# Kernel tuning notes

Hardware: AMD Instinct MI355X
Metric: run time of the kernel (lower is better)

Reference implementation:

```python
import jax, jax.numpy as jnp
import numpy as np

L, H, F_IN, OUT = 6, 2048, 2048, 2048
LN_EPS = 1e-5


def setup_inputs() -> dict:
    key = jax.random.key(0)
    ks = jax.random.split(key, 10)
    bound = 1.0 / np.sqrt(H)
    u = lambda k, shape: jax.random.uniform(k, shape, jnp.float32, -bound, bound)
    return {
        "x": jax.random.normal(ks[0], (1, 1, F_IN), jnp.float32),
        "hidden": jax.random.normal(ks[1], (L, 1, H), jnp.float32),
        "w_ih": u(ks[2], (L, 3 * H, H)),   # layer0 input size == H by construction
        "w_hh": u(ks[3], (L, 3 * H, H)),
        "b_ih": u(ks[4], (L, 3 * H)),
        "b_hh": u(ks[5], (L, 3 * H)),
        "ln_gamma": jnp.ones((H,), jnp.float32),
        "ln_beta": jnp.zeros((H,), jnp.float32),
        "lin_w": u(ks[6], (OUT, H)),
        "lin_b": u(ks[7], (OUT,)),
    }


def _gru_stack(x_t, hidden, w_ih, w_hh, b_ih, b_hh):
    # x_t: [B, H]; hidden: [L, B, H]. PyTorch gate order: r, z, n.
    def layer(inp, params):
        wi, wh, bi, bh, h = params
        gi = (inp @ wi.T + bi).reshape(inp.shape[0], 3, -1)  # [B,3,H]
        gh = (h @ wh.T + bh).reshape(h.shape[0], 3, -1)
        r = jax.nn.sigmoid(gi[:, 0] + gh[:, 0])
        z = jax.nn.sigmoid(gi[:, 1] + gh[:, 1])
        n = jnp.tanh(gi[:, 2] + r * gh[:, 2])
        h_new = (1.0 - z) * n + z * h
        return h_new, h_new

    top, new_hidden = jax.lax.scan(layer, x_t, (w_ih, w_hh, b_ih, b_hh, hidden))
    return top, new_hidden  # [B,H], [L,B,H]


def reference(x, hidden, w_ih, w_hh, b_ih, b_hh, ln_gamma, ln_beta, lin_w, lin_b):
    x_t = x[:, -1, :]  # [B, F_in]; T=1 so this is the only step
    out, new_hidden = _gru_stack(x_t, hidden, w_ih, w_hh, b_ih, b_hh)
    # LayerNorm over last dim
    mu = jnp.mean(out, axis=-1, keepdims=True)
    var = jnp.mean(jnp.square(out - mu), axis=-1, keepdims=True)
    out = (out - mu) * jax.lax.rsqrt(var + LN_EPS) * ln_gamma + ln_beta
    pred = out @ lin_w.T + lin_b + x_t[:, :OUT]
    return pred, new_hidden
```

## Files before the change

kernel.cpp:

```cpp
#include <hip/hip_runtime.h>


constexpr int HID = 2048;
constexpr int NL  = 6;
constexpr int G3  = 3 * HID;

__device__ __forceinline__ float wave_sum(float s){
  #pragma unroll
  for(int off = 32; off; off >>= 1) s += __shfl_down(s, off, 64);
  return s;
}

__device__ __forceinline__ float dot_f32(const float* __restrict__ row,
                                         const float* __restrict__ v, int lane){
  const float4* r4 = (const float4*)row;
  const float4* v4 = (const float4*)v;
  float s = 0.f;
  #pragma unroll
  for(int it = 0; it < 8; ++it){
    int idx = lane + 64 * it;
    float4 w = r4[idx], a = v4[idx];
    s += w.x * a.x + w.y * a.y + w.z * a.z + w.w * a.w;
  }
  return s;
}

__global__ __launch_bounds__(384) void k_layer(
    const float* __restrict__ w_ih_l,
    const float* __restrict__ w_hh_l,
    const float* __restrict__ b_ih_l,
    const float* __restrict__ b_hh_l,
    const float* __restrict__ h_l,
    const float* __restrict__ inp,
    float* __restrict__ h_new_ws,
    float* __restrict__ h_new_out)
{
  int j    = blockIdx.x;
  int wave = threadIdx.x >> 6;
  int lane = threadIdx.x & 63;
  __shared__ float sums[6];
  float s;
  if(wave < 3){
    s = dot_f32(w_ih_l + (size_t)(wave * HID + j) * HID, inp, lane);
  } else {
    s = dot_f32(w_hh_l + (size_t)((wave - 3) * HID + j) * HID, h_l, lane);
  }
  s = wave_sum(s);
  if(lane == 0) sums[wave] = s;
  __syncthreads();
  if(threadIdx.x == 0){
    float gi_r = sums[0] + b_ih_l[j];
    float gi_z = sums[1] + b_ih_l[HID + j];
    float gi_n = sums[2] + b_ih_l[2 * HID + j];
    float gh_r = sums[3] + b_hh_l[j];
    float gh_z = sums[4] + b_hh_l[HID + j];
    float gh_n = sums[5] + b_hh_l[2 * HID + j];
    float r = 1.f / (1.f + __expf(-(gi_r + gh_r)));
    float z = 1.f / (1.f + __expf(-(gi_z + gh_z)));
    float n = tanhf(gi_n + r * gh_n);
    float hn = (1.f - z) * n + z * h_l[j];
    h_new_ws[j]  = hn;
    h_new_out[j] = hn;
  }
}

__global__ __launch_bounds__(256) void k_layernorm(
    const float* __restrict__ h,
    const float* __restrict__ gamma,
    const float* __restrict__ beta,
    float* __restrict__ out)
{
  __shared__ float rs[4], rs2[4];
  __shared__ float s_mu, s_istd;
  int wave = threadIdx.x >> 6, lane = threadIdx.x & 63;
  float s = 0.f, s2 = 0.f;
  for(int i = threadIdx.x; i < HID; i += 256){ float v = h[i]; s += v; s2 += v * v; }
  #pragma unroll
  for(int off = 32; off; off >>= 1){ s += __shfl_down(s, off, 64); s2 += __shfl_down(s2, off, 64); }
  if(lane == 0){ rs[wave] = s; rs2[wave] = s2; }
  __syncthreads();
  if(threadIdx.x == 0){
    float S  = rs[0] + rs[1] + rs[2] + rs[3];
    float S2 = rs2[0] + rs2[1] + rs2[2] + rs2[3];
    float m   = S * (1.f / HID);
    float var = S2 * (1.f / HID) - m * m;
    s_mu = m; s_istd = rsqrtf(var + 1e-5f);
  }
  __syncthreads();
  float mu = s_mu, istd = s_istd;
  for(int i = threadIdx.x; i < HID; i += 256){
    out[i] = (h[i] - mu) * istd * gamma[i] + beta[i];
  }
}

__global__ __launch_bounds__(256) void k_linear(
    const float* __restrict__ v,
    const float* __restrict__ lin_w,
    const float* __restrict__ lin_b,
    const float* __restrict__ x,
    float* __restrict__ pred)
{
  int o    = blockIdx.x * 4 + (threadIdx.x >> 6);
  int lane = threadIdx.x & 63;
  float s = dot_f32(lin_w + (size_t)o * HID, v, lane);
  s = wave_sum(s);
  if(lane == 0) pred[o] = s + lin_b[o] + x[o];
}

extern "C" void kernel_launch(void* const* d_in, const int* in_sizes, int n_in,
                              void* d_out, int out_size, void* d_ws, size_t ws_size,
                              hipStream_t stream){
  const float* x      = (const float*)d_in[0];
  const float* hidden = (const float*)d_in[1];
  const float* w_ih   = (const float*)d_in[2];
  const float* w_hh   = (const float*)d_in[3];
  const float* b_ih   = (const float*)d_in[4];
  const float* b_hh   = (const float*)d_in[5];
  const float* gamma  = (const float*)d_in[6];
  const float* beta   = (const float*)d_in[7];
  const float* lin_w  = (const float*)d_in[8];
  const float* lin_b  = (const float*)d_in[9];
  float* out = (float*)d_out;

  float* buf = (float*)d_ws;

  for(int l = 0; l < NL; ++l){
    k_layer<<<HID, 384, 0, stream>>>(
        w_ih + (size_t)l * G3 * HID,
        w_hh + (size_t)l * G3 * HID,
        b_ih + (size_t)l * G3,
        b_hh + (size_t)l * G3,
        hidden + (size_t)l * HID,
        (l == 0) ? x : buf + (size_t)(l - 1) * HID,
        buf + (size_t)l * HID,
        out + HID + (size_t)l * HID);
  }
  k_layernorm<<<1, 256, 0, stream>>>(buf + 5 * HID, gamma, beta, buf + 6 * HID);
  k_linear<<<HID / 4, 256, 0, stream>>>(buf + 6 * HID, lin_w, lin_b, x, out);
}
```

Before: 603.0 us.

## Hoist all hidden-state matvecs out of the layer chain into one batched launch

All six layers' w_hh matvecs and layer 0's w_ih matvec are computed up front in a single large launch, since they depend only on the initial inputs. The sequential per-layer kernels then only stream w_ih and apply the gate math using the precomputed gh values. This moves most of the weight traffic off the serial dependency chain and into one highly parallel launch, aiming to improve memory bandwidth use. In exchange it adds a workspace buffer for gate pre-activations and an extra small cell kernel for layer 0.

```diff
diff --git a/kernel.cpp b/kernel.cpp
--- a/kernel.cpp
+++ b/kernel.cpp
@@ -1,9 +1,10 @@
 #include <hip/hip_runtime.h>
 
 
-constexpr int HID = 2048;
-constexpr int NL  = 6;
-constexpr int G3  = 3 * HID;
+constexpr int HID  = 2048;
+constexpr int G3   = 3 * HID;
+constexpr int NGH  = 6 * G3;
+constexpr int NROW = NGH + G3;
 
 __device__ __forceinline__ float wave_sum(float s){
   #pragma unroll
@@ -25,42 +26,78 @@
   return s;
 }
 
-__global__ __launch_bounds__(384) void k_layer(
+__device__ __forceinline__ float sigm(float v){ return 1.f / (1.f + __expf(-v)); }
+
+__global__ __launch_bounds__(512) void k_par_matvec(
+    const float* __restrict__ w_ih,
+    const float* __restrict__ w_hh,
+    const float* __restrict__ b_ih,
+    const float* __restrict__ b_hh,
+    const float* __restrict__ x,
+    const float* __restrict__ hidden,
+    float* __restrict__ gh_all,
+    float* __restrict__ gi0)
+{
+  int t    = blockIdx.x * 8 + (threadIdx.x >> 6);
+  int lane = threadIdx.x & 63;
+  if(t >= NROW) return;
+  const float *row, *v;
+  float bias; float* dst;
+  if(t < NGH){
+    int l = t / G3, r = t % G3;
+    row  = w_hh + ((size_t)l * G3 + r) * HID;
+    v    = hidden + l * HID;
+    bias = b_hh[l * G3 + r];
+    dst  = gh_all + l * G3 + r;
+  } else {
+    int r = t - NGH;
+    row  = w_ih + (size_t)r * HID;
+    v    = x;
+    bias = b_ih[r];
+    dst  = gi0 + r;
+  }
+  float s = wave_sum(dot_f32(row, v, lane));
+  if(lane == 0) *dst = s + bias;
+}
+
+__global__ __launch_bounds__(256) void k_cell0(
+    const float* __restrict__ gi0, const float* __restrict__ gh0,
+    const float* __restrict__ h_orig,
+    float* __restrict__ h_ws, float* __restrict__ h_out)
+{
+  int j = blockIdx.x * 256 + threadIdx.x;
+  float r  = sigm(gi0[j] + gh0[j]);
+  float z  = sigm(gi0[HID + j] + gh0[HID + j]);
+  float n  = tanhf(gi0[2 * HID + j] + r * gh0[2 * HID + j]);
+  float hn = (1.f - z) * n + z * h_orig[j];
+  h_ws[j] = hn; h_out[j] = hn;
+}
+
+__global__ __launch_bounds__(384) void k_gi_cell(
     const float* __restrict__ w_ih_l,
-    const float* __restrict__ w_hh_l,
     const float* __restrict__ b_ih_l,
-    const float* __restrict__ b_hh_l,
-    const float* __restrict__ h_l,
+    const float* __restrict__ gh_l,
+    const float* __restrict__ h_orig,
     const float* __restrict__ inp,
-    float* __restrict__ h_new_ws,
-    float* __restrict__ h_new_out)
+    float* __restrict__ h_ws, float* __restrict__ h_out)
 {
-  int j    = blockIdx.x;
-  int wave = threadIdx.x >> 6;
-  int lane = threadIdx.x & 63;
-  __shared__ float sums[6];
-  float s;
-  if(wave < 3){
-    s = dot_f32(w_ih_l + (size_t)(wave * HID + j) * HID, inp, lane);
-  } else {
-    s = dot_f32(w_hh_l + (size_t)((wave - 3) * HID + j) * HID, h_l, lane);
-  }
-  s = wave_sum(s);
-  if(lane == 0) sums[wave] = s;
+  int half  = threadIdx.x >= 192;
+  int gate  = (threadIdx.x >> 6) % 3;
+  int lane  = threadIdx.x & 63;
+  int j     = blockIdx.x * 2 + half;
+  __shared__ float sums[2][3];
+  float s = wave_sum(dot_f32(w_ih_l + ((size_t)gate * HID + j) * HID, inp, lane));
+  if(lane == 0) sums[half][gate] = s;
   __syncthreads();
-  if(threadIdx.x == 0){
-    float gi_r = sums[0] + b_ih_l[j];
-    float gi_z = sums[1] + b_ih_l[HID + j];
-    float gi_n = sums[2] + b_ih_l[2 * HID + j];
-    float gh_r = sums[3] + b_hh_l[j];
-    float gh_z = sums[4] + b_hh_l[HID + j];
-    float gh_n = sums[5] + b_hh_l[2 * HID + j];
-    float r = 1.f / (1.f + __expf(-(gi_r + gh_r)));
-    float z = 1.f / (1.f + __expf(-(gi_z + gh_z)));
-    float n = tanhf(gi_n + r * gh_n);
-    float hn = (1.f - z) * n + z * h_l[j];
-    h_new_ws[j]  = hn;
-    h_new_out[j] = hn;
+  if(lane == 0 && gate == 0){
+    float gi_r = sums[half][0] + b_ih_l[j];
+    float gi_z = sums[half][1] + b_ih_l[HID + j];
+    float gi_n = sums[half][2] + b_ih_l[2 * HID + j];
+    float r  = sigm(gi_r + gh_l[j]);
+    float z  = sigm(gi_z + gh_l[HID + j]);
+    float n  = tanhf(gi_n + r * gh_l[2 * HID + j]);
+    float hn = (1.f - z) * n + z * h_orig[j];
+    h_ws[j] = hn; h_out[j] = hn;
   }
 }
 
@@ -102,8 +139,7 @@
 {
   int o    = blockIdx.x * 4 + (threadIdx.x >> 6);
   int lane = threadIdx.x & 63;
-  float s = dot_f32(lin_w + (size_t)o * HID, v, lane);
-  s = wave_sum(s);
+  float s = wave_sum(dot_f32(lin_w + (size_t)o * HID, v, lane));
   if(lane == 0) pred[o] = s + lin_b[o] + x[o];
 }
 
@@ -122,19 +158,28 @@
   const float* lin_b  = (const float*)d_in[9];
   float* out = (float*)d_out;
 
-  float* buf = (float*)d_ws;
+  float* buf     = (float*)d_ws;
+  float* gh_all  = buf;
+  float* gi0     = buf + NGH;
+  float* h_chain = buf + NROW;
+  float* ln_out  = buf + NROW + 6*HID;
 
-  for(int l = 0; l < NL; ++l){
-    k_layer<<<HID, 384, 0, stream>>>(
+  k_par_matvec<<<(NROW + 7) / 8, 512, 0, stream>>>(
+      w_ih, w_hh, b_ih, b_hh, x, hidden, gh_all, gi0);
+
+  k_cell0<<<HID / 256, 256, 0, stream>>>(gi0, gh_all, hidden, h_chain, out + HID);
+
+  for(int l = 1; l < 6; ++l){
+    k_gi_cell<<<HID / 2, 384, 0, stream>>>(
         w_ih + (size_t)l * G3 * HID,
-        w_hh + (size_t)l * G3 * HID,
         b_ih + (size_t)l * G3,
-        b_hh + (size_t)l * G3,
+        gh_all + (size_t)l * G3,
         hidden + (size_t)l * HID,
-        (l == 0) ? x : buf + (size_t)(l - 1) * HID,
-        buf + (size_t)l * HID,
+        h_chain + (size_t)(l - 1) * HID,
+        h_chain + (size_t)l * HID,
         out + HID + (size_t)l * HID);
   }
-  k_layernorm<<<1, 256, 0, stream>>>(buf + 5 * HID, gamma, beta, buf + 6 * HID);
-  k_linear<<<HID / 4, 256, 0, stream>>>(buf + 6 * HID, lin_w, lin_b, x, out);
+
+  k_layernorm<<<1, 256, 0, stream>>>(h_chain + 5 * HID, gamma, beta, ln_out);
+  k_linear<<<HID / 4, 256, 0, stream>>>(ln_out, lin_w, lin_b, x, out);
 }
```

After: 606.5 us. No clear change (+0.6%).
